# Kernel tuning notes

Measured on AMD Instinct MI355X. Metric: run time of the kernel, lower is better.

Reference implementation:

```python
import jax, jax.numpy as jnp
import numpy as np

VOCAB = 32000
D = 256
B, S = 16, 128


def setup_inputs() -> dict:
    key = jax.random.key(0)
    ks = jax.random.split(key, 8)
    s = 1.0 / np.sqrt(D)
    return {
        "X": jax.random.randint(ks[0], (B, S), 0, VOCAB),
        "emb": jax.random.normal(ks[1], (VOCAB, D), dtype=jnp.float32),
        "Wl": jax.random.uniform(ks[2], (D, D), jnp.float32, -s, s),
        "bl": jax.random.uniform(ks[3], (D,), jnp.float32, -s, s),
        "Wr": jax.random.uniform(ks[4], (D, D), jnp.float32, -s, s),
        "br": jax.random.uniform(ks[5], (D,), jnp.float32, -s, s),
        "Wrel": jax.random.uniform(ks[6], (D, D), jnp.float32, -s, s),
        "brel": jax.random.uniform(ks[7], (D,), jnp.float32, -s, s),
    }


def reference(X, emb, Wl, bl, Wr, br, Wrel, brel):
    # X: [B,S] int -> embed [B,S,D]
    e = emb[X]
    L = jnp.einsum("bsd,de->bse", e, Wl.T) + bl  # left projection per token
    R = jnp.einsum("bsd,de->bse", e, Wr.T) + br  # right projection per token
    # all-pairs relu(L_i + R_j): [B,S,S,D]
    pair = jax.nn.relu(L[:, :, None, :] + R[:, None, :, :])
    # relation is affine, so mean over S^2 pairs commutes with it (same math,
    # one [B,D] GEMM instead of B*S^2 tiny ones)
    pooled = pair.mean(axis=(1, 2))  # [B,D]
    return pooled @ Wrel.T + brel
```

## Files before the change

kernel.cpp:

```cpp
#include <hip/hip_runtime.h>
#include <hip/hip_bf16.h>

#define DD 256
#define SS 128
#define BB 16

typedef __attribute__((ext_vector_type(8))) short bf16x8;
typedef __attribute__((ext_vector_type(4))) short bf16x4;
typedef __attribute__((ext_vector_type(4))) float f32x4;

static __device__ __forceinline__ short f2bf(float f) {
    __hip_bfloat16 h = __float2bfloat16(f);
    return *reinterpret_cast<short*>(&h);
}

static __device__ __forceinline__ int swz(int r, int kb) {
    return r * 512 + (kb ^ ((r & 7) << 4));
}


__global__ __launch_bounds__(512, 2) void k_fused(
    const int* __restrict__ X, const float* __restrict__ emb,
    const float* __restrict__ Wl, const float* __restrict__ bl,
    const float* __restrict__ Wr, const float* __restrict__ br,
    float* __restrict__ sumLg, float* __restrict__ sumRg,
    float* __restrict__ absS)
{
    __shared__ __align__(16) short Ebf[128 * 256];
    __shared__ __align__(16) float Lcol[16 * 132];
    __shared__ __align__(16) float Rcol[16 * 132];
    __shared__ float redA[512];
    __shared__ float redwL[8 * 16];
    __shared__ float redwR[8 * 16];
    __shared__ int toksh[SS];

    const int tid  = threadIdx.x;
    const int bx   = (blockIdx.x & 7) * 32 + (blockIdx.x >> 3);
    const int b    = bx >> 4;
    const int dc   = bx & 15;
    const int dr0  = dc * 16;
    const int w    = tid >> 6;
    const int lane = tid & 63;
    const int lr   = lane & 15, lk = lane >> 4;
    const int c4   = tid & 63;

    if (tid < SS) toksh[tid] = X[b * SS + tid];
    __syncthreads();

    char* Eb = (char*)Ebf;

    float4 ga[8];
#pragma unroll
    for (int i = 0; i < 8; ++i)
        ga[i] = *(const float4*)&emb[(size_t)toksh[i * 8 + w] * DD + c4 * 4];

    bf16x8 wlf[8], wrf[8];
    {
        const float* plw = Wl + (size_t)(dr0 + lr) * DD + lk * 8;
        const float* prw = Wr + (size_t)(dr0 + lr) * DD + lk * 8;
#pragma unroll
        for (int ks = 0; ks < 8; ++ks) {
            float4 f0 = *(const float4*)(plw + ks * 32);
            float4 f1 = *(const float4*)(plw + ks * 32 + 4);
            bf16x8 p;
            p[0]=f2bf(f0.x); p[1]=f2bf(f0.y); p[2]=f2bf(f0.z); p[3]=f2bf(f0.w);
            p[4]=f2bf(f1.x); p[5]=f2bf(f1.y); p[6]=f2bf(f1.z); p[7]=f2bf(f1.w);
            wlf[ks] = p;
            f0 = *(const float4*)(prw + ks * 32);
            f1 = *(const float4*)(prw + ks * 32 + 4);
            p[0]=f2bf(f0.x); p[1]=f2bf(f0.y); p[2]=f2bf(f0.z); p[3]=f2bf(f0.w);
            p[4]=f2bf(f1.x); p[5]=f2bf(f1.y); p[6]=f2bf(f1.z); p[7]=f2bf(f1.w);
            wrf[ks] = p;
        }
    }

#pragma unroll
    for (int i = 0; i < 8; ++i) {
        bf16x4 p; p[0]=f2bf(ga[i].x); p[1]=f2bf(ga[i].y); p[2]=f2bf(ga[i].z); p[3]=f2bf(ga[i].w);
        *(bf16x4*)(Eb + swz(i * 8 + w, c4 * 8)) = p;
    }
#pragma unroll
    for (int i = 0; i < 8; ++i)
        ga[i] = *(const float4*)&emb[(size_t)toksh[64 + i * 8 + w] * DD + c4 * 4];
#pragma unroll
    for (int i = 0; i < 8; ++i) {
        bf16x4 p; p[0]=f2bf(ga[i].x); p[1]=f2bf(ga[i].y); p[2]=f2bf(ga[i].z); p[3]=f2bf(ga[i].w);
        *(bf16x4*)(Eb + swz(64 + i * 8 + w, c4 * 8)) = p;
    }
    __syncthreads();

    f32x4 accL = {0.f,0.f,0.f,0.f}, accR = accL;
#pragma unroll
    for (int ks = 0; ks < 8; ++ks) {
        bf16x8 a = *(bf16x8*)(Eb + swz(w * 16 + lr, ks * 64 + lk * 16));
        accL = __builtin_amdgcn_mfma_f32_16x16x32_bf16(a, wlf[ks], accL, 0, 0, 0);
        accR = __builtin_amdgcn_mfma_f32_16x16x32_bf16(a, wrf[ks], accR, 0, 0, 0);
    }
    const float blv = bl[dr0 + lr];
    const float brv = br[dr0 + lr];
#pragma unroll
    for (int reg = 0; reg < 4; ++reg) {
        int s = w * 16 + lk * 4 + reg;
        Lcol[lr * 132 + s] = accL[reg] + blv;
        Rcol[lr * 132 + s] = accR[reg] + brv;
    }
    float tl = (accL[0] + accL[1]) + (accL[2] + accL[3]) + blv * 4.0f;
    float tr = (accR[0] + accR[1]) + (accR[2] + accR[3]) + brv * 4.0f;
    tl += __shfl_xor(tl, 16);  tr += __shfl_xor(tr, 16);
    tl += __shfl_xor(tl, 32);  tr += __shfl_xor(tr, 32);
    if (lane < 16) { redwL[w * 16 + lr] = tl; redwR[w * 16 + lr] = tr; }
    __syncthreads();

    const int d = tid & 15, jg = tid >> 4;
    float rr[4];
    *(float4*)rr = *(float4*)&Rcol[d * 132 + jg * 4];

    float a0 = 0.f, a1 = 0.f, a2 = 0.f, a3 = 0.f;
    for (int i = 0; i < 128; i += 4) {
        float4 l4 = *(float4*)&Lcol[d * 132 + i];
#pragma unroll
        for (int q = 0; q < 4; ++q) {
            a0 += fabsf(l4.x + rr[q]);
            a1 += fabsf(l4.y + rr[q]);
            a2 += fabsf(l4.z + rr[q]);
            a3 += fabsf(l4.w + rr[q]);
        }
    }
    redA[tid] = (a0 + a1) + (a2 + a3);
    __syncthreads();

    if (tid < 16) {
        float sa = 0.f;
#pragma unroll
        for (int g = 0; g < 32; ++g) sa += redA[g * 16 + tid];
        float sl = 0.f, sr = 0.f;
#pragma unroll
        for (int wv = 0; wv < 8; ++wv) {
            sl += redwL[wv * 16 + tid];
            sr += redwR[wv * 16 + tid];
        }
        absS [b * DD + dr0 + tid] = sa;
        sumLg[b * DD + dr0 + tid] = sl;
        sumRg[b * DD + dr0 + tid] = sr;
    }
}

__global__ __launch_bounds__(256) void k_final(
    const float* __restrict__ sumLg, const float* __restrict__ sumRg,
    const float* __restrict__ absS,
    const float* __restrict__ Wrel, const float* __restrict__ brel,
    float* __restrict__ out)
{
    __shared__ float plds[DD];
    const int tid = threadIdx.x;
    const int b   = blockIdx.x;

    float sl = sumLg[b * DD + tid];
    float sr = sumRg[b * DD + tid];
    float sa = absS [b * DD + tid];

    plds[tid] = (128.0f * (sl + sr) + sa) * (1.0f / 32768.0f);
    __syncthreads();

    float acc = brel[tid];
    const float4* w4 = (const float4*)(Wrel + (size_t)tid * DD);
#pragma unroll
    for (int k4 = 0; k4 < DD / 4; ++k4) {
        float4 p = *(float4*)&plds[k4 * 4];
        float4 w = w4[k4];
        acc = fmaf(p.x, w.x, acc);
        acc = fmaf(p.y, w.y, acc);
        acc = fmaf(p.z, w.z, acc);
        acc = fmaf(p.w, w.w, acc);
    }
    out[b * DD + tid] = acc;
}

extern "C" void kernel_launch(void* const* d_in, const int* in_sizes, int n_in,
                              void* d_out, int out_size, void* d_ws, size_t ws_size,
                              hipStream_t stream) {
    const int*   X    = (const int*)d_in[0];
    const float* emb  = (const float*)d_in[1];
    const float* Wl   = (const float*)d_in[2];
    const float* bl   = (const float*)d_in[3];
    const float* Wr   = (const float*)d_in[4];
    const float* br   = (const float*)d_in[5];
    const float* Wrel = (const float*)d_in[6];
    const float* brel = (const float*)d_in[7];
    float* out = (float*)d_out;

    float* ws    = (float*)d_ws;
    float* sumLg = ws;
    float* sumRg = sumLg + BB * DD;
    float* absS  = sumRg + BB * DD;

    k_fused<<<BB * 16, 512, 0, stream>>>(X, emb, Wl, bl, Wr, br,
                                         sumLg, sumRg, absS);
    k_final<<<BB, 256, 0, stream>>>(sumLg, sumRg, absS, Wrel, brel, out);
}
```

Measured before the change: 28.28 us.

## Merge final GEMV into fused kernel via cooperative grid sync

Folds the small final projection kernel into the main kernel, using a cooperative launch and a grid-wide sync so the first 16 blocks compute the output after all partial sums are written. This is meant to remove the second kernel launch and the gap between the two kernels. In exchange it adds a grid barrier over 256 blocks and the overhead of a cooperative launch, and it depends on all blocks being co-resident.

```diff
diff --git a/kernel.cpp b/kernel.cpp
--- a/kernel.cpp
+++ b/kernel.cpp
@@ -1,5 +1,8 @@
 #include <hip/hip_runtime.h>
 #include <hip/hip_bf16.h>
+#include <hip/hip_cooperative_groups.h>
+
+namespace cg = cooperative_groups;
 
 #define DD 256
 #define SS 128
@@ -19,12 +22,13 @@
 }
 
 
-__global__ __launch_bounds__(512, 2) void k_fused(
+__global__ __launch_bounds__(512, 2) void k_all(
     const int* __restrict__ X, const float* __restrict__ emb,
     const float* __restrict__ Wl, const float* __restrict__ bl,
     const float* __restrict__ Wr, const float* __restrict__ br,
+    const float* __restrict__ Wrel, const float* __restrict__ brel,
     float* __restrict__ sumLg, float* __restrict__ sumRg,
-    float* __restrict__ absS)
+    float* __restrict__ absS, float* __restrict__ out)
 {
     __shared__ __align__(16) short Ebf[128 * 256];
     __shared__ __align__(16) float Lcol[16 * 132];
@@ -143,37 +147,34 @@
         sumLg[b * DD + dr0 + tid] = sl;
         sumRg[b * DD + dr0 + tid] = sr;
     }
-}
-
-__global__ __launch_bounds__(256) void k_final(
-    const float* __restrict__ sumLg, const float* __restrict__ sumRg,
-    const float* __restrict__ absS,
-    const float* __restrict__ Wrel, const float* __restrict__ brel,
-    float* __restrict__ out)
-{
-    __shared__ float plds[DD];
-    const int tid = threadIdx.x;
-    const int b   = blockIdx.x;
-
-    float sl = sumLg[b * DD + tid];
-    float sr = sumRg[b * DD + tid];
-    float sa = absS [b * DD + tid];
-
-    plds[tid] = (128.0f * (sl + sr) + sa) * (1.0f / 32768.0f);
-    __syncthreads();
-
-    float acc = brel[tid];
-    const float4* w4 = (const float4*)(Wrel + (size_t)tid * DD);
-#pragma unroll
-    for (int k4 = 0; k4 < DD / 4; ++k4) {
-        float4 p = *(float4*)&plds[k4 * 4];
-        float4 w = w4[k4];
-        acc = fmaf(p.x, w.x, acc);
-        acc = fmaf(p.y, w.y, acc);
-        acc = fmaf(p.z, w.z, acc);
-        acc = fmaf(p.w, w.w, acc);
-    }
-    out[b * DD + tid] = acc;
+
+    cg::this_grid().sync();
+
+    if (blockIdx.x < BB) {
+        const int fb = blockIdx.x;
+        float* pooled = redA;
+        if (tid < DD) {
+            float sl = sumLg[fb * DD + tid];
+            float sr = sumRg[fb * DD + tid];
+            float sa = absS [fb * DD + tid];
+            pooled[tid] = (128.0f * (sl + sr) + sa) * (1.0f / 32768.0f);
+        }
+        __syncthreads();
+        if (tid < DD) {
+            float acc = brel[tid];
+            const float4* w4 = (const float4*)(Wrel + (size_t)tid * DD);
+#pragma unroll
+            for (int k4 = 0; k4 < DD / 4; ++k4) {
+                float4 p = *(float4*)&pooled[k4 * 4];
+                float4 wv = w4[k4];
+                acc = fmaf(p.x, wv.x, acc);
+                acc = fmaf(p.y, wv.y, acc);
+                acc = fmaf(p.z, wv.z, acc);
+                acc = fmaf(p.w, wv.w, acc);
+            }
+            out[fb * DD + tid] = acc;
+        }
+    }
 }
 
 extern "C" void kernel_launch(void* const* d_in, const int* in_sizes, int n_in,
@@ -194,7 +195,9 @@
     float* sumRg = sumLg + BB * DD;
     float* absS  = sumRg + BB * DD;
 
-    k_fused<<<BB * 16, 512, 0, stream>>>(X, emb, Wl, bl, Wr, br,
-                                         sumLg, sumRg, absS);
-    k_final<<<BB, 256, 0, stream>>>(sumLg, sumRg, absS, Wrel, brel, out);
-}
+    void* args[] = { (void*)&X, (void*)&emb, (void*)&Wl, (void*)&bl,
+                     (void*)&Wr, (void*)&br, (void*)&Wrel, (void*)&brel,
+                     (void*)&sumLg, (void*)&sumRg, (void*)&absS, (void*)&out };
+    hipLaunchCooperativeKernel((void*)k_all, dim3(BB * 16), dim3(512),
+                               args, 0, stream);
+}
```

New measurement: 63.92 us. 2.26x slower.
